# Kernel optimization log

Hardware: AMD Instinct MI355X
Metric: run time of the kernel (lower is better)

Reference implementation:

```python
import jax, jax.numpy as jnp
import numpy as np

N_NODES = 100000
N_EDGES = 1600000
IN_CH = 128
HID = 128   # 2 * out_channels
OUT = 64


def setup_inputs() -> dict:
    key = jax.random.key(0)
    ks = jax.random.split(key, 5)
    x = jax.random.normal(ks[0], (N_NODES, IN_CH), dtype=jnp.float32)
    edge_index = jax.random.randint(ks[1], (2, N_EDGES), 0, N_NODES, dtype=jnp.int64)
    # Glorot-ish init for the two GCN weight matrices
    W1 = jax.random.normal(ks[2], (IN_CH, HID), dtype=jnp.float32) / np.sqrt(IN_CH)
    b1 = jnp.zeros((HID,), dtype=jnp.float32)
    W2 = jax.random.normal(ks[3], (HID, OUT), dtype=jnp.float32) / np.sqrt(HID)
    b2 = jnp.zeros((OUT,), dtype=jnp.float32)
    return {"x": x, "edge_index": edge_index, "W1": W1, "b1": b1, "W2": W2, "b2": b2}


def _gcn_conv(x, W, b, src, dst, coef, n):
    # Standard GCNConv: D^{-1/2} (A + I) D^{-1/2} X W + b
    xw = x @ W                                   # [N, F_out]
    msg = xw[src] * coef[:, None]                # gather + scale  [E+N, F_out]
    agg = jax.ops.segment_sum(msg, dst, num_segments=n)  # scatter-add [N, F_out]
    return agg + b


def reference(x, edge_index, W1, b1, W2, b2):
    n = x.shape[0]
    loops = jnp.arange(n, dtype=edge_index.dtype)
    src = jnp.concatenate([edge_index[0], loops])  # add self loops
    dst = jnp.concatenate([edge_index[1], loops])
    deg = jax.ops.segment_sum(jnp.ones_like(src, dtype=x.dtype), dst, num_segments=n)
    dinv = jnp.where(deg > 0, jax.lax.rsqrt(deg), 0.0)
    coef = dinv[src] * dinv[dst]                  # symmetric normalization per edge

    h = _gcn_conv(x, W1, b1, src, dst, coef, n)
    h = jax.nn.relu(h)                            # non_linearity=True
    # F.normalize(p=2, dim=-1) with eps clamp 1e-12; dropout inactive (eval mode)
    h = h / jnp.maximum(jnp.linalg.norm(h, axis=-1, keepdims=True), 1e-12)
    return _gcn_conv(h, W2, b2, src, dst, coef, n)
```

## Files before the change

kernel.cpp:

```cpp
#include <hip/hip_runtime.h>
#include <hip/hip_bf16.h>


#define IN_CH 128
#define HID 128
#define OUT_CH 64
#define NBLK 128
#define MAXNB 1568

typedef unsigned int uint_t;
typedef unsigned short ushort_t;
typedef __attribute__((ext_vector_type(8))) short bf16x8;
typedef __attribute__((ext_vector_type(4))) float f32x4;

__device__ __forceinline__ ushort_t f32_to_bf16_rn(float f) {
    uint_t u = __float_as_uint(f);
    u = (u + 0x7fffu + ((u >> 16) & 1u)) >> 16;
    return (ushort_t)u;
}
__device__ __forceinline__ float bf16lo_to_f32(uint_t u) { return __uint_as_float(u << 16); }
__device__ __forceinline__ float bf16hi_to_f32(uint_t u) { return __uint_as_float(u & 0xffff0000u); }

__global__ __launch_bounds__(256) void hist_kernel(const int* __restrict__ dst, int E,
                                                   int chunk, int NB,
                                                   int* __restrict__ blk_cnt) {
    __shared__ int hist[MAXNB];
    int tid = threadIdx.x;
    int blk = blockIdx.x;
    for (int b = tid; b < NB; b += 256) hist[b] = 0;
    __syncthreads();
    int start = blk * chunk;
    int end = start + chunk; if (end > E) end = E;
    int e = start + tid;
    for (; e + 768 < end; e += 1024) {
        int d0 = dst[e], d1 = dst[e + 256], d2 = dst[e + 512], d3 = dst[e + 768];
        atomicAdd(&hist[d0 >> 6], 1);
        atomicAdd(&hist[d1 >> 6], 1);
        atomicAdd(&hist[d2 >> 6], 1);
        atomicAdd(&hist[d3 >> 6], 1);
    }
    for (; e < end; e += 256) atomicAdd(&hist[dst[e] >> 6], 1);
    __syncthreads();
    for (int b = tid; b < NB; b += 256) blk_cnt[blk * NB + b] = hist[b];
}

__global__ __launch_bounds__(256) void btot_kernel(const int* __restrict__ blk_cnt,
                                                   int NB, int* __restrict__ btot) {
    int b = blockIdx.x * 256 + threadIdx.x;
    if (b < NB) {
        int sum = 0;
        #pragma unroll 8
        for (int blk = 0; blk < NBLK; blk++) sum += blk_cnt[blk * NB + b];
        btot[b] = sum;
    }
}

__global__ __launch_bounds__(256) void scan_kernel(const int* __restrict__ btot, int NB,
                                                   int* __restrict__ bucket_base,
                                                   int* __restrict__ row_start,
                                                   int n, int E) {
    __shared__ int sdata[256];
    __shared__ int carryS;
    int tid = threadIdx.x;
    if (tid == 0) carryS = 0;
    __syncthreads();
    int nchunks = (NB + 255) / 256;
    for (int c = 0; c < nchunks; c++) {
        int i = c * 256 + tid;
        int v = (i < NB) ? btot[i] : 0;
        sdata[tid] = v;
        __syncthreads();
        for (int off = 1; off < 256; off <<= 1) {
            int t = (tid >= off) ? sdata[tid - off] : 0;
            __syncthreads();
            sdata[tid] += t;
            __syncthreads();
        }
        if (i < NB) bucket_base[i] = carryS + sdata[tid] - v;
        __syncthreads();
        if (tid == 0) carryS += sdata[255];
        __syncthreads();
    }
    if (tid == 0) {
        bucket_base[NB] = E;
        row_start[n] = E;
    }
}

__global__ __launch_bounds__(256) void colscan_kernel(const int* __restrict__ blk_cnt,
                                                      const int* __restrict__ bucket_base,
                                                      int NB, int* __restrict__ blk_start) {
    __shared__ int tile[NBLK][16];
    int tid = threadIdx.x;
    int b0 = blockIdx.x * 16;
    for (int idx = tid; idx < NBLK * 16; idx += 256) {
        int blk = idx >> 4, b = idx & 15;
        if (b0 + b < NB) tile[blk][b] = blk_cnt[blk * NB + b0 + b];
    }
    __syncthreads();
    if (tid < 16 && b0 + tid < NB) {
        int running = bucket_base[b0 + tid];
        for (int blk = 0; blk < NBLK; blk++) {
            int t = tile[blk][tid];
            tile[blk][tid] = running;
            running += t;
        }
    }
    __syncthreads();
    for (int idx = tid; idx < NBLK * 16; idx += 256) {
        int blk = idx >> 4, b = idx & 15;
        if (b0 + b < NB) blk_start[blk * NB + b0 + b] = tile[blk][b];
    }
}

__global__ __launch_bounds__(256) void scatter_kernel(const int* __restrict__ src,
                                                      const int* __restrict__ dst,
                                                      int E, int chunk, int NB,
                                                      const int* __restrict__ blk_start,
                                                      uint_t* __restrict__ pairs) {
    __shared__ int cur[MAXNB];
    int tid = threadIdx.x;
    int blk = blockIdx.x;
    for (int b = tid; b < NB; b += 256) cur[b] = blk_start[blk * NB + b];
    __syncthreads();
    int start = blk * chunk;
    int end = start + chunk; if (end > E) end = E;
    int e = start + tid;
    for (; e + 768 < end; e += 1024) {
        int d0 = dst[e], d1 = dst[e + 256], d2 = dst[e + 512], d3 = dst[e + 768];
        int s0 = src[e], s1 = src[e + 256], s2 = src[e + 512], s3 = src[e + 768];
        int p0 = atomicAdd(&cur[d0 >> 6], 1);
        int p1 = atomicAdd(&cur[d1 >> 6], 1);
        int p2 = atomicAdd(&cur[d2 >> 6], 1);
        int p3 = atomicAdd(&cur[d3 >> 6], 1);
        pairs[p0] = (uint_t)s0 | ((uint_t)(d0 & 63) << 26);
        pairs[p1] = (uint_t)s1 | ((uint_t)(d1 & 63) << 26);
        pairs[p2] = (uint_t)s2 | ((uint_t)(d2 & 63) << 26);
        pairs[p3] = (uint_t)s3 | ((uint_t)(d3 & 63) << 26);
    }
    for (; e < end; e += 256) {
        int d = dst[e], s = src[e];
        int p = atomicAdd(&cur[d >> 6], 1);
        pairs[p] = (uint_t)s | ((uint_t)(d & 63) << 26);
    }
}

__global__ __launch_bounds__(256) void fine_fill_kernel(const uint_t* __restrict__ pairs,
                                                        const int* __restrict__ bucket_base,
                                                        int* __restrict__ row_start,
                                                        float* __restrict__ dinv,
                                                        int* __restrict__ csr_src,
                                                        int n) {
    __shared__ int cnt64[64];
    __shared__ int cur[64];
    int b = blockIdx.x;
    int node0 = b << 6;
    int tid = threadIdx.x;
    if (tid < 64) cnt64[tid] = 0;
    __syncthreads();
    int start = bucket_base[b];
    int end = bucket_base[b + 1];
    int e = start + tid;
    for (; e + 768 < end; e += 1024) {
        uint_t u0 = pairs[e], u1 = pairs[e + 256], u2 = pairs[e + 512], u3 = pairs[e + 768];
        atomicAdd(&cnt64[u0 >> 26], 1);
        atomicAdd(&cnt64[u1 >> 26], 1);
        atomicAdd(&cnt64[u2 >> 26], 1);
        atomicAdd(&cnt64[u3 >> 26], 1);
    }
    for (; e < end; e += 256) atomicAdd(&cnt64[pairs[e] >> 26], 1);
    __syncthreads();
    if (tid < 64) {
        int c = cnt64[tid];
        int v = c;
        #pragma unroll
        for (int off = 1; off < 64; off <<= 1) {
            int u = __shfl_up(v, off, 64);
            if (tid >= off) v += u;
        }
        int excl = start + v - c;
        if (node0 + tid < n) {
            row_start[node0 + tid] = excl;
            dinv[node0 + tid] = rsqrtf((float)(c + 1));
        }
        cur[tid] = excl;
    }
    __syncthreads();
    e = start + tid;
    for (; e + 768 < end; e += 1024) {
        uint_t u0 = pairs[e], u1 = pairs[e + 256], u2 = pairs[e + 512], u3 = pairs[e + 768];
        int p0 = atomicAdd(&cur[u0 >> 26], 1);
        int p1 = atomicAdd(&cur[u1 >> 26], 1);
        int p2 = atomicAdd(&cur[u2 >> 26], 1);
        int p3 = atomicAdd(&cur[u3 >> 26], 1);
        csr_src[p0] = (int)(u0 & 0x3FFFFFFu);
        csr_src[p1] = (int)(u1 & 0x3FFFFFFu);
        csr_src[p2] = (int)(u2 & 0x3FFFFFFu);
        csr_src[p3] = (int)(u3 & 0x3FFFFFFu);
    }
    for (; e < end; e += 256) {
        uint_t u = pairs[e];
        int p = atomicAdd(&cur[u >> 26], 1);
        csr_src[p] = (int)(u & 0x3FFFFFFu);
    }
}

__global__ __launch_bounds__(256) void wsplit_kernel(const float* __restrict__ W1,
                                                     const float* __restrict__ W2,
                                                     ushort_t* __restrict__ w1h,
                                                     ushort_t* __restrict__ w1l,
                                                     ushort_t* __restrict__ w2h,
                                                     ushort_t* __restrict__ w2l) {
    int idx = blockIdx.x * 256 + threadIdx.x;
    const int tot1 = 128 * 128;
    const int tot = tot1 + 64 * 128;
    if (idx >= tot) return;
    float v;
    ushort_t* ph;
    ushort_t* pl;
    int o;
    if (idx < tot1) {
        int c = idx >> 7, k = idx & 127;
        v = W1[k * 128 + c];
        ph = w1h; pl = w1l; o = idx;
    } else {
        int j = idx - tot1;
        int c = j >> 7, k = j & 127;
        v = W2[k * 64 + c];
        ph = w2h; pl = w2l; o = j;
    }
    ushort_t h = f32_to_bf16_rn(v);
    float hv = __uint_as_float((uint_t)h << 16);
    ph[o] = h;
    pl[o] = f32_to_bf16_rn(v - hv);
}

template <int NCOL, bool F32_IN>
__global__ __launch_bounds__(256) void mfma_gemm_kernel(const void* __restrict__ Xv,
                                                        const ushort_t* __restrict__ Wth,
                                                        const ushort_t* __restrict__ Wtl,
                                                        const float* __restrict__ rowscale,
                                                        ushort_t* __restrict__ Y, int n) {
    constexpr int NT = NCOL / 16;
    const float* X = (const float*)Xv;
    const ushort_t* Hb = (const ushort_t*)Xv;

    int tid = threadIdx.x;
    int wave = tid >> 6;
    int lane = tid & 63;
    int q = lane >> 4;
    int r16 = lane & 15;
    int rowBase = blockIdx.x * 64 + wave * 16;
    int arow = rowBase + r16;
    if (arow > n - 1) arow = n - 1;

    f32x4 acc[NT];
    #pragma unroll
    for (int t = 0; t < NT; t++) acc[t] = (f32x4){0.f, 0.f, 0.f, 0.f};

    #pragma unroll
    for (int ks = 0; ks < 4; ks++) {
        int k0 = ks * 32 + q * 8;
        bf16x8 ah, al = {};
        if (F32_IN) {
            const float4* xr = (const float4*)(X + (size_t)arow * 128 + k0);
            float4 p0 = xr[0], p1 = xr[1];
            float v[8] = {p0.x, p0.y, p0.z, p0.w, p1.x, p1.y, p1.z, p1.w};
            #pragma unroll
            for (int j = 0; j < 8; j++) {
                ushort_t hb = f32_to_bf16_rn(v[j]);
                float hv = __uint_as_float((uint_t)hb << 16);
                ah[j] = (short)hb;
                al[j] = (short)f32_to_bf16_rn(v[j] - hv);
            }
        } else {
            ah = *(const bf16x8*)(Hb + (size_t)arow * 128 + k0);
        }
        #pragma unroll
        for (int t = 0; t < NT; t++) {
            size_t wo = (size_t)(t * 16 + r16) * 128 + k0;
            bf16x8 bh = *(const bf16x8*)(Wth + wo);
            bf16x8 bl = *(const bf16x8*)(Wtl + wo);
            acc[t] = __builtin_amdgcn_mfma_f32_16x16x32_bf16(ah, bh, acc[t], 0, 0, 0);
            acc[t] = __builtin_amdgcn_mfma_f32_16x16x32_bf16(ah, bl, acc[t], 0, 0, 0);
            if (F32_IN)
                acc[t] = __builtin_amdgcn_mfma_f32_16x16x32_bf16(al, bh, acc[t], 0, 0, 0);
        }
    }

    #pragma unroll
    for (int rr = 0; rr < 4; rr++) {
        int row = rowBase + q * 4 + rr;
        if (row < n) {
            float rs = rowscale[row];
            #pragma unroll
            for (int t = 0; t < NT; t++)
                Y[(size_t)row * NCOL + t * 16 + r16] = f32_to_bf16_rn(acc[t][rr] * rs);
        }
    }
}

__global__ __launch_bounds__(256) void agg1_kernel(const ushort_t* __restrict__ xw,
                                                   const int* __restrict__ csr_src,
                                                   const int* __restrict__ row_start,
                                                   const float* __restrict__ dinv,
                                                   const float* __restrict__ b1,
                                                   ushort_t* __restrict__ h, int n) {
    int wid = (blockIdx.x * 256 + threadIdx.x) >> 6;
    int lane = threadIdx.x & 63;
    if (wid >= n) return;
    int i = wid;
    float di = dinv[i];
    int e0 = row_start[i], e1 = row_start[i + 1];
    uint_t su = ((const uint_t*)(xw + (size_t)i * HID))[lane];
    float ax = bf16lo_to_f32(su), ay = bf16hi_to_f32(su);
    int e = e0;
    for (; e + 8 <= e1; e += 8) {
        int s[8];
        #pragma unroll
        for (int j = 0; j < 8; j++) s[j] = csr_src[e + j];
        uint_t v[8];
        #pragma unroll
        for (int j = 0; j < 8; j++)
            v[j] = ((const uint_t*)(xw + (size_t)s[j] * HID))[lane];
        #pragma unroll
        for (int j = 0; j < 8; j++) {
            ax += bf16lo_to_f32(v[j]);
            ay += bf16hi_to_f32(v[j]);
        }
    }
    if (e < e1) {
        int last = e1 - 1;
        int s[8];
        #pragma unroll
        for (int j = 0; j < 8; j++) {
            int idx = e + j;
            s[j] = csr_src[idx <= last ? idx : last];
        }
        uint_t v[8];
        #pragma unroll
        for (int j = 0; j < 8; j++)
            v[j] = ((const uint_t*)(xw + (size_t)s[j] * HID))[lane];
        #pragma unroll
        for (int j = 0; j < 8; j++) {
            float c = (e + j <= last) ? 1.0f : 0.0f;
            ax = fmaf(bf16lo_to_f32(v[j]), c, ax);
            ay = fmaf(bf16hi_to_f32(v[j]), c, ay);
        }
    }
    ax = fmaf(ax, di, b1[lane * 2]);
    ay = fmaf(ay, di, b1[lane * 2 + 1]);
    ax = fmaxf(ax, 0.f);
    ay = fmaxf(ay, 0.f);
    float ss = ax * ax + ay * ay;
    #pragma unroll
    for (int m = 32; m >= 1; m >>= 1) ss += __shfl_xor(ss, m, 64);
    float scale = 1.0f / fmaxf(sqrtf(ss), 1e-12f);
    uint_t u = (uint_t)f32_to_bf16_rn(ax * scale) |
               ((uint_t)f32_to_bf16_rn(ay * scale) << 16);
    ((uint_t*)(h + (size_t)i * HID))[lane] = u;
}

__global__ __launch_bounds__(256) void agg2_kernel(const ushort_t* __restrict__ hw,
                                                   const int* __restrict__ csr_src,
                                                   const int* __restrict__ row_start,
                                                   const float* __restrict__ dinv,
                                                   const float* __restrict__ b2,
                                                   float* __restrict__ out, int n) {
    int wid = (blockIdx.x * 256 + threadIdx.x) >> 6;
    int lane = threadIdx.x & 63;
    int i = wid * 2 + (lane >> 5);
    int l = lane & 31;
    if (i >= n) return;
    float di = dinv[i];
    uint_t su = ((const uint_t*)(hw + (size_t)i * OUT_CH))[l];
    float ax = bf16lo_to_f32(su), ay = bf16hi_to_f32(su);
    int e0 = row_start[i], e1 = row_start[i + 1];
    int e = e0;
    for (; e + 8 <= e1; e += 8) {
        int s[8];
        #pragma unroll
        for (int j = 0; j < 8; j++) s[j] = csr_src[e + j];
        uint_t v[8];
        #pragma unroll
        for (int j = 0; j < 8; j++)
            v[j] = ((const uint_t*)(hw + (size_t)s[j] * OUT_CH))[l];
        #pragma unroll
        for (int j = 0; j < 8; j++) {
            ax += bf16lo_to_f32(v[j]);
            ay += bf16hi_to_f32(v[j]);
        }
    }
    if (e < e1) {
        int last = e1 - 1;
        int s[8];
        #pragma unroll
        for (int j = 0; j < 8; j++) {
            int idx = e + j;
            s[j] = csr_src[idx <= last ? idx : last];
        }
        uint_t v[8];
        #pragma unroll
        for (int j = 0; j < 8; j++)
            v[j] = ((const uint_t*)(hw + (size_t)s[j] * OUT_CH))[l];
        #pragma unroll
        for (int j = 0; j < 8; j++) {
            float c = (e + j <= last) ? 1.0f : 0.0f;
            ax = fmaf(bf16lo_to_f32(v[j]), c, ax);
            ay = fmaf(bf16hi_to_f32(v[j]), c, ay);
        }
    }
    ax = fmaf(ax, di, b2[l * 2]);
    ay = fmaf(ay, di, b2[l * 2 + 1]);
    ((float2*)(out + (size_t)i * OUT_CH))[l] = make_float2(ax, ay);
}

extern "C" void kernel_launch(void* const* d_in, const int* in_sizes, int n_in,
                              void* d_out, int out_size, void* d_ws, size_t ws_size,
                              hipStream_t stream) {
    const float* x  = (const float*)d_in[0];
    const int*   ei = (const int*)d_in[1];
    const float* W1 = (const float*)d_in[2];
    const float* b1 = (const float*)d_in[3];
    const float* W2 = (const float*)d_in[4];
    const float* b2 = (const float*)d_in[5];
    float* out = (float*)d_out;

    const int N = in_sizes[0] / IN_CH;
    const int E = in_sizes[1] / 2;
    const int* src = ei;
    const int* dst = ei + E;
    const int NB = (N + 63) / 64;
    const int chunk = (E + NBLK - 1) / NBLK;

    char* base = (char*)d_ws;
    size_t off = 0;
    auto alloc = [&](size_t bytes) -> void* {
        void* p = base + off;
        off = (off + bytes + 255) & ~(size_t)255;
        return p;
    };
    int*      blk_cnt     = (int*)alloc((size_t)NBLK * NB * 4);
    int*      blk_start   = (int*)alloc((size_t)NBLK * NB * 4);
    int*      btot        = (int*)alloc((size_t)NB * 4);
    int*      bucket_base = (int*)alloc((size_t)(NB + 1) * 4);
    int*      row_start   = (int*)alloc((size_t)(N + 1) * 4);
    float*    dinv        = (float*)alloc((size_t)N * 4);
    int*      csr_src     = (int*)alloc((size_t)E * 4);
    uint_t*   pairs       = (uint_t*)alloc((size_t)E * 4);
    ushort_t* xw          = (ushort_t*)alloc((size_t)N * HID * 2);
    ushort_t* h           = (ushort_t*)alloc((size_t)N * HID * 2);
    ushort_t* hw          = (ushort_t*)alloc((size_t)N * OUT_CH * 2);
    ushort_t* w1h         = (ushort_t*)alloc((size_t)128 * 128 * 2);
    ushort_t* w1l         = (ushort_t*)alloc((size_t)128 * 128 * 2);
    ushort_t* w2h         = (ushort_t*)alloc((size_t)64 * 128 * 2);
    ushort_t* w2l         = (ushort_t*)alloc((size_t)64 * 128 * 2);
    (void)ws_size;

    wsplit_kernel<<<(128 * 128 + 64 * 128 + 255) / 256, 256, 0, stream>>>(
        W1, W2, w1h, w1l, w2h, w2l);

    hist_kernel<<<NBLK, 256, 0, stream>>>(dst, E, chunk, NB, blk_cnt);
    btot_kernel<<<(NB + 255) / 256, 256, 0, stream>>>(blk_cnt, NB, btot);
    scan_kernel<<<1, 256, 0, stream>>>(btot, NB, bucket_base, row_start, N, E);
    colscan_kernel<<<(NB + 15) / 16, 256, 0, stream>>>(blk_cnt, bucket_base, NB, blk_start);
    scatter_kernel<<<NBLK, 256, 0, stream>>>(src, dst, E, chunk, NB, blk_start, pairs);
    fine_fill_kernel<<<NB, 256, 0, stream>>>(pairs, bucket_base, row_start, dinv,
                                             csr_src, N);

    mfma_gemm_kernel<128, true><<<(N + 63) / 64, 256, 0, stream>>>(
        x, w1h, w1l, dinv, xw, N);
    agg1_kernel<<<(N * 64 + 255) / 256, 256, 0, stream>>>(xw, csr_src, row_start,
                                                          dinv, b1, h, N);
    mfma_gemm_kernel<64, false><<<(N + 63) / 64, 256, 0, stream>>>(
        h, w2h, w2l, dinv, hw, N);
    int waves2 = (N + 1) / 2;
    agg2_kernel<<<(waves2 * 64 + 255) / 256, 256, 0, stream>>>(hw, csr_src, row_start,
                                                               dinv, b2, out, N);
}
```

Baseline: 346.8 us.

## Stage split weights in LDS and compute two row tiles per wave in GEMM

```diff
diff --git a/kernel.cpp b/kernel.cpp
--- a/kernel.cpp
+++ b/kernel.cpp
@@ -236,66 +236,95 @@
 }
 
 template <int NCOL, bool F32_IN>
-__global__ __launch_bounds__(256) void mfma_gemm_kernel(const void* __restrict__ Xv,
-                                                        const ushort_t* __restrict__ Wth,
-                                                        const ushort_t* __restrict__ Wtl,
-                                                        const float* __restrict__ rowscale,
-                                                        ushort_t* __restrict__ Y, int n) {
+__global__ __launch_bounds__(256, 2) void mfma_gemm_kernel(const void* __restrict__ Xv,
+                                                           const ushort_t* __restrict__ Wth,
+                                                           const ushort_t* __restrict__ Wtl,
+                                                           const float* __restrict__ rowscale,
+                                                           ushort_t* __restrict__ Y, int n) {
     constexpr int NT = NCOL / 16;
-    const float* X = (const float*)Xv;
-    const ushort_t* Hb = (const ushort_t*)Xv;
+    constexpr int WB = NCOL * 128 * 2;
+    constexpr int NCH = WB / 16;
+    __shared__ __align__(16) char Bs[2 * WB];
 
     int tid = threadIdx.x;
+
+    for (int i = tid; i < 2 * NCH; i += 256) {
+        bool lo = (i >= NCH);
+        int j = lo ? i - NCH : i;
+        int row = j >> 4, c = j & 15;
+        bf16x8 v = *(const bf16x8*)((lo ? Wtl : Wth) + row * 128 + c * 8);
+        int bo = (row << 8) + (c << 4);
+        bo ^= (row & 7) << 4;
+        *(bf16x8*)(Bs + (lo ? WB : 0) + bo) = v;
+    }
+    __syncthreads();
+
     int wave = tid >> 6;
     int lane = tid & 63;
     int q = lane >> 4;
     int r16 = lane & 15;
-    int rowBase = blockIdx.x * 64 + wave * 16;
-    int arow = rowBase + r16;
-    if (arow > n - 1) arow = n - 1;
-
-    f32x4 acc[NT];
+    int rowBase = blockIdx.x * 128 + wave * 32;
+    int ar0 = rowBase + r16;      if (ar0 > n - 1) ar0 = n - 1;
+    int ar1 = rowBase + 16 + r16; if (ar1 > n - 1) ar1 = n - 1;
+
+    const float* X = (const float*)Xv;
+    const ushort_t* Hb = (const ushort_t*)Xv;
+
+    f32x4 acc[2][NT];
     #pragma unroll
-    for (int t = 0; t < NT; t++) acc[t] = (f32x4){0.f, 0.f, 0.f, 0.f};
+    for (int rt = 0; rt < 2; rt++)
+        #pragma unroll
+        for (int t = 0; t < NT; t++) acc[rt][t] = (f32x4){0.f, 0.f, 0.f, 0.f};
 
     #pragma unroll
     for (int ks = 0; ks < 4; ks++) {
         int k0 = ks * 32 + q * 8;
-        bf16x8 ah, al = {};
-        if (F32_IN) {
-            const float4* xr = (const float4*)(X + (size_t)arow * 128 + k0);
-            float4 p0 = xr[0], p1 = xr[1];
-            float v[8] = {p0.x, p0.y, p0.z, p0.w, p1.x, p1.y, p1.z, p1.w};
+        bf16x8 ah[2], al[2] = {};
+        #pragma unroll
+        for (int rt = 0; rt < 2; rt++) {
+            int arow = rt ? ar1 : ar0;
+            if (F32_IN) {
+                const float4* xr = (const float4*)(X + (size_t)arow * 128 + k0);
+                float4 p0 = xr[0], p1 = xr[1];
+                float v[8] = {p0.x, p0.y, p0.z, p0.w, p1.x, p1.y, p1.z, p1.w};
+                #pragma unroll
+                for (int j = 0; j < 8; j++) {
+                    ushort_t hb = f32_to_bf16_rn(v[j]);
+                    float hv = __uint_as_float((uint_t)hb << 16);
+                    ah[rt][j] = (short)hb;
+                    al[rt][j] = (short)f32_to_bf16_rn(v[j] - hv);
+                }
+            } else {
+                ah[rt] = *(const bf16x8*)(Hb + (size_t)arow * 128 + k0);
+            }
+        }
+        #pragma unroll
+        for (int t = 0; t < NT; t++) {
+            int bo = ((t * 16 + r16) << 8) + ks * 64 + (q << 4);
+            bo ^= (r16 & 7) << 4;
+            bf16x8 bh = *(const bf16x8*)(Bs + bo);
+            bf16x8 bl = *(const bf16x8*)(Bs + WB + bo);
             #pragma unroll
-            for (int j = 0; j < 8; j++) {
-                ushort_t hb = f32_to_bf16_rn(v[j]);
-                float hv = __uint_as_float((uint_t)hb << 16);
-                ah[j] = (short)hb;
-                al[j] = (short)f32_to_bf16_rn(v[j] - hv);
+            for (int rt = 0; rt < 2; rt++) {
+                acc[rt][t] = __builtin_amdgcn_mfma_f32_16x16x32_bf16(ah[rt], bh, acc[rt][t], 0, 0, 0);
+                acc[rt][t] = __builtin_amdgcn_mfma_f32_16x16x32_bf16(ah[rt], bl, acc[rt][t], 0, 0, 0);
+                if (F32_IN)
+                    acc[rt][t] = __builtin_amdgcn_mfma_f32_16x16x32_bf16(al[rt], bh, acc[rt][t], 0, 0, 0);
             }
-        } else {
-            ah = *(const bf16x8*)(Hb + (size_t)arow * 128 + k0);
-        }
-        #pragma unroll
-        for (int t = 0; t < NT; t++) {
-            size_t wo = (size_t)(t * 16 + r16) * 128 + k0;
-            bf16x8 bh = *(const bf16x8*)(Wth + wo);
-            bf16x8 bl = *(const bf16x8*)(Wtl + wo);
-            acc[t] = __builtin_amdgcn_mfma_f32_16x16x32_bf16(ah, bh, acc[t], 0, 0, 0);
-            acc[t] = __builtin_amdgcn_mfma_f32_16x16x32_bf16(ah, bl, acc[t], 0, 0, 0);
-            if (F32_IN)
-                acc[t] = __builtin_amdgcn_mfma_f32_16x16x32_bf16(al, bh, acc[t], 0, 0, 0);
         }
     }
 
     #pragma unroll
-    for (int rr = 0; rr < 4; rr++) {
-        int row = rowBase + q * 4 + rr;
-        if (row < n) {
-            float rs = rowscale[row];
-            #pragma unroll
-            for (int t = 0; t < NT; t++)
-                Y[(size_t)row * NCOL + t * 16 + r16] = f32_to_bf16_rn(acc[t][rr] * rs);
+    for (int rt = 0; rt < 2; rt++) {
+        #pragma unroll
+        for (int rr = 0; rr < 4; rr++) {
+            int row = rowBase + rt * 16 + q * 4 + rr;
+            if (row < n) {
+                float rs = rowscale[row];
+                #pragma unroll
+                for (int t = 0; t < NT; t++)
+                    Y[(size_t)row * NCOL + t * 16 + r16] = f32_to_bf16_rn(acc[rt][t][rr] * rs);
+            }
         }
     }
 }
@@ -468,11 +497,11 @@
     fine_fill_kernel<<<NB, 256, 0, stream>>>(pairs, bucket_base, row_start, dinv,
                                              csr_src, N);
 
-    mfma_gemm_kernel<128, true><<<(N + 63) / 64, 256, 0, stream>>>(
+    mfma_gemm_kernel<128, true><<<(N + 127) / 128, 256, 0, stream>>>(
         x, w1h, w1l, dinv, xw, N);
     agg1_kernel<<<(N * 64 + 255) / 256, 256, 0, stream>>>(xw, csr_src, row_start,
                                                           dinv, b1, h, N);
-    mfma_gemm_kernel<64, false><<<(N + 63) / 64, 256, 0, stream>>>(
+    mfma_gemm_kernel<64, false><<<(N + 127) / 128, 256, 0, stream>>>(
         h, w2h, w2l, dinv, hw, N);
     int waves2 = (N + 1) / 2;
     agg2_kernel<<<(waves2 * 64 + 255) / 256, 256, 0, stream>>>(hw, csr_src, row_start,
```

Result: faster. 291.7 us (-15.9%).
